# Kernel tuning notes

Measured on AMD Instinct MI355X. Metric: run time of the kernel, lower is better.

The kernel has to match this reference:

```python
import jax, jax.numpy as jnp
import numpy as np

B, S, D = 8, 2048, 512
KD = 64          # key_dim == value_dim
WIDTH = 128      # attention_width
NEG = 1.0e9


def setup_inputs() -> dict:
    key = jax.random.key(0)
    ks = jax.random.split(key, 16)
    glorot_dd = float(np.sqrt(6.0 / (D + KD)))
    glorot_sd = float(np.sqrt(6.0 / (S + KD)))
    u = lambda k, shape, lim: jax.random.uniform(k, shape, jnp.float32, -lim, lim)
    return {
        "x": jax.random.normal(ks[0], (B, S, D), jnp.float32),
        "Wqr": u(ks[1], (D, KD), glorot_dd), "bqr": jnp.zeros((KD,), jnp.float32),
        "Wqi": u(ks[2], (D, KD), glorot_dd), "bqi": jnp.zeros((KD,), jnp.float32),
        "Wkr": u(ks[3], (D, KD), glorot_dd), "bkr": jnp.zeros((KD,), jnp.float32),
        "Wki": u(ks[4], (D, KD), glorot_dd), "bki": jnp.zeros((KD,), jnp.float32),
        "Wv": u(ks[5], (D, KD), glorot_dd),  "bv": jnp.zeros((KD,), jnp.float32),
        "pos_qr": u(ks[6], (S, KD), glorot_sd), "pos_qi": u(ks[7], (S, KD), glorot_sd),
        "pos_kr": u(ks[8], (S, KD), glorot_sd), "pos_ki": u(ks[9], (S, KD), glorot_sd),
        "temperature": jnp.ones((1,), jnp.float32),
    }


def _masks():
    ind = jnp.arange(S)
    band = (jnp.abs(ind[:, None] - ind[None, :]) <= WIDTH).astype(jnp.float32)  # [S,S]
    causal = jnp.tril(jnp.ones((S, S), jnp.float32))                            # [S,S]
    return band, causal


def reference(x, Wqr, bqr, Wqi, bqi, Wkr, bkr, Wki, bki, Wv, bv,
              pos_qr, pos_qi, pos_kr, pos_ki, temperature):
    scale = 1.0 / jnp.sqrt(jnp.float32(KD))
    # complex Q/K via two real Dense layers; Q scaled BEFORE adding interference
    qr = (x @ Wqr + bqr) * scale + pos_qr[None]   # [B,S,KD]
    qi = (x @ Wqi + bqi) * scale + pos_qi[None]
    kr = (x @ Wkr + bkr) + pos_kr[None]
    ki = (x @ Wki + bki) + pos_ki[None]
    v = x @ Wv + bv                                # [B,S,KD]
    # real part of complex Q @ K^T (transpose, not conjugate-transpose)
    scores = (jnp.einsum('bsd,btd->bst', qr, kr)
              - jnp.einsum('bsd,btd->bst', qi, ki)) * scale  # [B,S,S]
    band, causal = _masks()
    scores = scores * band - NEG * (1.0 - band)
    scores = scores * causal - NEG * (1.0 - causal)
    probs = jax.nn.softmax(scores * temperature[0], axis=-1)
    return jnp.einsum('bst,btd->bsd', probs, v)
```

## Files before the change

kernel.cpp:

```cpp
#include <hip/hip_runtime.h>

#define NB 8
#define NS 2048
#define ND 512
#define NKD 64
#define NM (NB*NS)

typedef _Float16 f16x8 __attribute__((ext_vector_type(8)));
typedef float f32x4 __attribute__((ext_vector_type(4)));


__global__ __launch_bounds__(256) void wprep_kernel(
    const float* __restrict__ w0, const float* __restrict__ w1,
    const float* __restrict__ w2, const float* __restrict__ w3,
    const float* __restrict__ w4,
    f16x8* __restrict__ wfrag)
{
    const int t = blockIdx.x * 256 + threadIdx.x;
    const int p    = t >> 12;
    const int nf   = (t >> 10) & 3;
    const int kt   = (t >> 6) & 15;
    const int lane = t & 63;
    const float* __restrict__ W = (p==0)?w0:(p==1)?w1:(p==2)?w2:(p==3)?w3:w4;
    const int n  = nf*16 + (lane & 15);
    const int k0 = kt*32 + (lane >> 4)*8;
    f16x8 v;
    #pragma unroll
    for (int j = 0; j < 8; ++j)
        v[j] = (_Float16)W[(size_t)(k0 + j)*NKD + n];
    wfrag[t] = v;
}

__global__ __launch_bounds__(256) void proj_mfma(
    const float* __restrict__ x,
    const f16x8* __restrict__ wfrag,
    const float* __restrict__ b0, const float* __restrict__ b1,
    const float* __restrict__ b2, const float* __restrict__ b3,
    const float* __restrict__ b4,
    const float* __restrict__ p0, const float* __restrict__ p1,
    const float* __restrict__ p2, const float* __restrict__ p3,
    _Float16* __restrict__ qkri,
    _Float16* __restrict__ vT)
{
    const int g    = (blockIdx.x * 256 + threadIdx.x) >> 6;
    const int lane = threadIdx.x & 63;
    const int m0   = g * 16;

    const int row = m0 + (lane & 15);
    const int kb  = (lane >> 4) * 8;
    const float* __restrict__ xrow = x + (size_t)row * ND + kb;
    const f16x8* __restrict__ wf   = wfrag + lane;

    f32x4 acc[5][4];
    #pragma unroll
    for (int p = 0; p < 5; ++p)
        #pragma unroll
        for (int nf = 0; nf < 4; ++nf) acc[p][nf] = (f32x4){0.f,0.f,0.f,0.f};

    for (int kt = 0; kt < 16; ++kt) {
        float4 xa = *(const float4*)(xrow + kt*32);
        float4 xb = *(const float4*)(xrow + kt*32 + 4);
        f16x8 a;
        a[0]=(_Float16)xa.x; a[1]=(_Float16)xa.y;
        a[2]=(_Float16)xa.z; a[3]=(_Float16)xa.w;
        a[4]=(_Float16)xb.x; a[5]=(_Float16)xb.y;
        a[6]=(_Float16)xb.z; a[7]=(_Float16)xb.w;
        #pragma unroll
        for (int p = 0; p < 5; ++p)
            #pragma unroll
            for (int nf = 0; nf < 4; ++nf) {
                f16x8 b = wf[(p*4 + nf)*1024 + kt*64];
                acc[p][nf] = __builtin_amdgcn_mfma_f32_16x16x32_f16(a, b, acc[p][nf], 0, 0, 0);
            }
    }

    const float* biases[5] = {b0, b1, b2, b3, b4};
    const float* poss[4]   = {p0, p1, p2, p3};

    const int col   = lane & 15;
    const int rbase = (lane >> 4) << 2;
    const int bidx  = m0 >> 11;

    #pragma unroll
    for (int p = 0; p < 4; ++p) {
        _Float16* ob = qkri + ((size_t)p*NM + m0) * NKD;
        #pragma unroll
        for (int nf = 0; nf < 4; ++nf) {
            const int c = nf*16 + col;
            const float bb = biases[p][c];
            #pragma unroll
            for (int r = 0; r < 4; ++r) {
                const int mm = rbase + r;
                const int s  = (m0 + mm) & (NS - 1);
                float t = acc[p][nf][r] + bb;
                if (p < 2) t = t * 0.125f + poss[p][s*NKD + c];
                else       t = t + poss[p][s*NKD + c];
                ob[(size_t)mm*NKD + c] = (_Float16)t;
            }
        }
    }
    {
        _Float16* vb = vT + (size_t)bidx*NKD*NS;
        #pragma unroll
        for (int nf = 0; nf < 4; ++nf) {
            const int c = nf*16 + col;
            const float bb = b4[c];
            #pragma unroll
            for (int r = 0; r < 4; ++r) {
                const int s = (m0 + rbase + r) & (NS - 1);
                vb[(size_t)c*NS + s] = (_Float16)(acc[4][nf][r] + bb);
            }
        }
    }
}

#define SST 164
#define OST 68

__global__ __launch_bounds__(256) void attn_mfma(
    const _Float16* __restrict__ qkri,
    const _Float16* __restrict__ vT,
    const float* __restrict__ temp,
    float* __restrict__ out)
{
    __shared__ __align__(16) float scf[16*SST];
    __shared__ __align__(16) float olds[3][16*OST];

    const int tid  = threadIdx.x;
    const int w    = tid >> 6;
    const int lane = tid & 63;
    const int i0   = blockIdx.x * 16;
    const int b    = blockIdx.y;
    const int jb   = i0 - 128;

    const _Float16* __restrict__ qr_g = qkri + ((size_t)0*NM + (size_t)b*NS)*NKD;
    const _Float16* __restrict__ qi_g = qkri + ((size_t)1*NM + (size_t)b*NS)*NKD;
    const _Float16* __restrict__ kr_g = qkri + ((size_t)2*NM + (size_t)b*NS)*NKD;
    const _Float16* __restrict__ ki_g = qkri + ((size_t)3*NM + (size_t)b*NS)*NKD;
    const _Float16* __restrict__ vT_b = vT + (size_t)b*NKD*NS;

    const f16x8 zf = {};
    const int col  = lane & 15;
    const int seg  = lane >> 4;
    const int qg4  = seg * 4;

    const int qrow = i0 + col;
    const int d0   = seg * 8;
    f16x8 aqr[2], aqi[2];
    #pragma unroll
    for (int kt = 0; kt < 2; ++kt) {
        aqr[kt] = *(const f16x8*)&qr_g[(size_t)qrow*NKD + kt*32 + d0];
        f16x8 qi8 = *(const f16x8*)&qi_g[(size_t)qrow*NKD + kt*32 + d0];
        aqi[kt] = -qi8;
    }

    const float sT  = 0.125f * temp[0];
    const int jrmin = -jb;
    const int tA = (w == 0) ? 0 : (2*w + 1);
    const int tB = 2*w + 2;

    for (int t = tA; t <= tB; ++t) {
        const int row = jb + 16*t + col;
        const bool ok = (row >= 0);
        const _Float16* krp = kr_g + (size_t)row*NKD + d0;
        const _Float16* kip = ki_g + (size_t)row*NKD + d0;
        f16x8 bkr0 = ok ? *(const f16x8*)(krp)      : zf;
        f16x8 bkr1 = ok ? *(const f16x8*)(krp + 32) : zf;
        f16x8 bki0 = ok ? *(const f16x8*)(kip)      : zf;
        f16x8 bki1 = ok ? *(const f16x8*)(kip + 32) : zf;
        f32x4 acc = (f32x4){0.f,0.f,0.f,0.f};
        acc = __builtin_amdgcn_mfma_f32_16x16x32_f16(aqr[0], bkr0, acc, 0,0,0);
        acc = __builtin_amdgcn_mfma_f32_16x16x32_f16(aqr[1], bkr1, acc, 0,0,0);
        acc = __builtin_amdgcn_mfma_f32_16x16x32_f16(aqi[0], bki0, acc, 0,0,0);
        acc = __builtin_amdgcn_mfma_f32_16x16x32_f16(aqi[1], bki1, acc, 0,0,0);
        const int jr = 16*t + col;
        #pragma unroll
        for (int r = 0; r < 4; ++r) {
            const int row16 = qg4 + r;
            const bool okm = (jr >= row16) && (jr <= 128 + row16) && (jr >= jrmin);
            scf[(qg4 + r)*SST + jr] = okm ? acc[r]*sT : -1e30f;
        }
    }
    if (w == 0) {
        #pragma unroll
        for (int r = 0; r < 4; ++r)
            scf[(qg4 + r)*SST + 144 + col] = -1e30f;
    }
    __syncthreads();

    const float* srow = &scf[col*SST + seg*40];
    float4 vv[10];
    float m = -3e38f;
    #pragma unroll
    for (int c = 0; c < 10; ++c) {
        vv[c] = *(const float4*)(srow + 4*c);
        m = fmaxf(m, fmaxf(fmaxf(vv[c].x, vv[c].y), fmaxf(vv[c].z, vv[c].w)));
    }
    m = fmaxf(m, __shfl_xor(m, 16));
    m = fmaxf(m, __shfl_xor(m, 32));
    float l = 0.f;
    #pragma unroll
    for (int c = 0; c < 10; ++c) {
        l += __expf(vv[c].x - m) + __expf(vv[c].y - m)
           + __expf(vv[c].z - m) + __expf(vv[c].w - m);
    }
    l += __shfl_xor(l, 16);
    l += __shfl_xor(l, 32);
    const float inv = 1.0f / l;

    f32x4 oacc[4];
    #pragma unroll
    for (int nf = 0; nf < 4; ++nf) oacc[nf] = (f32x4){0.f,0.f,0.f,0.f};

    #pragma unroll
    for (int pass = 0; pass < 2; ++pass) {
        const int kt = (pass == 0) ? w : 4;
        if (pass == 1 && w != 0) break;
        const int sb = 32*kt + seg*8;
        float4 e0 = *(const float4*)&scf[col*SST + sb];
        float4 e1 = *(const float4*)&scf[col*SST + sb + 4];
        f16x8 a;
        a[0] = (_Float16)(__expf(e0.x - m) * inv);
        a[1] = (_Float16)(__expf(e0.y - m) * inv);
        a[2] = (_Float16)(__expf(e0.z - m) * inv);
        a[3] = (_Float16)(__expf(e0.w - m) * inv);
        a[4] = (_Float16)(__expf(e1.x - m) * inv);
        a[5] = (_Float16)(__expf(e1.y - m) * inv);
        a[6] = (_Float16)(__expf(e1.z - m) * inv);
        a[7] = (_Float16)(__expf(e1.w - m) * inv);
        const int k0 = jb + 32*kt + seg*8;
        const bool okv = (k0 >= 0) && (k0 <= NS - 8);
        #pragma unroll
        for (int nf = 0; nf < 4; ++nf) {
            const int d = nf*16 + col;
            f16x8 bv = okv ? *(const f16x8*)&vT_b[(size_t)d*NS + k0] : zf;
            oacc[nf] = __builtin_amdgcn_mfma_f32_16x16x32_f16(a, bv, oacc[nf], 0,0,0);
        }
    }

    if (w > 0) {
        #pragma unroll
        for (int nf = 0; nf < 4; ++nf)
            #pragma unroll
            for (int r = 0; r < 4; ++r)
                olds[w-1][(qg4 + r)*OST + nf*16 + col] = oacc[nf][r];
    }
    __syncthreads();
    if (w == 0) {
        float* ob = out + ((size_t)b*NS + i0)*NKD;
        #pragma unroll
        for (int nf = 0; nf < 4; ++nf)
            #pragma unroll
            for (int r = 0; r < 4; ++r) {
                const int idx = (qg4 + r)*OST + nf*16 + col;
                const float v = oacc[nf][r] + olds[0][idx] + olds[1][idx] + olds[2][idx];
                ob[(size_t)(qg4 + r)*NKD + nf*16 + col] = v;
            }
    }
}

extern "C" void kernel_launch(void* const* d_in, const int* in_sizes, int n_in,
                              void* d_out, int out_size, void* d_ws, size_t ws_size,
                              hipStream_t stream)
{
    const float* x    = (const float*)d_in[0];
    const float* w0   = (const float*)d_in[1];
    const float* b0   = (const float*)d_in[2];
    const float* w1   = (const float*)d_in[3];
    const float* b1   = (const float*)d_in[4];
    const float* w2   = (const float*)d_in[5];
    const float* b2   = (const float*)d_in[6];
    const float* w3   = (const float*)d_in[7];
    const float* b3   = (const float*)d_in[8];
    const float* w4   = (const float*)d_in[9];
    const float* b4   = (const float*)d_in[10];
    const float* p0   = (const float*)d_in[11];
    const float* p1   = (const float*)d_in[12];
    const float* p2   = (const float*)d_in[13];
    const float* p3   = (const float*)d_in[14];
    const float* temp = (const float*)d_in[15];

    char* ws = (char*)d_ws;
    f16x8*    wfrag = (f16x8*)ws;
    _Float16* qkri  = (_Float16*)(ws + 327680);
    _Float16* vT    = (_Float16*)(ws + 327680 + 8388608);

    wprep_kernel<<<80, 256, 0, stream>>>(w0, w1, w2, w3, w4, wfrag);

    proj_mfma<<<256, 256, 0, stream>>>(x, wfrag,
                                       b0, b1, b2, b3, b4,
                                       p0, p1, p2, p3, qkri, vT);

    dim3 gB(NS/16, NB);
    attn_mfma<<<gB, 256, 0, stream>>>(qkri, vT, temp, (float*)d_out);
}
```

Before: 43.77 us.

## Split projection outputs across wave pairs and stage V transpose through LDS

Each 16-row tile is now handled by two waves, each computing two of the four Q/K projections plus half of V. This halves per-wave accumulators and MFMA work and doubles the grid to 512 blocks for more parallelism. The V outputs are written to a shared-memory tile and then stored to vT as contiguous 16-byte vectors, replacing scattered 2-byte transposed stores. In exchange, x is loaded and converted twice per tile, and the block gains LDS use and a barrier.

```diff
diff --git a/kernel.cpp b/kernel.cpp
--- a/kernel.cpp
+++ b/kernel.cpp
@@ -42,20 +42,28 @@
     _Float16* __restrict__ qkri,
     _Float16* __restrict__ vT)
 {
-    const int g    = (blockIdx.x * 256 + threadIdx.x) >> 6;
+    __shared__ __align__(16) _Float16 vtile[64][40];
+
+    const int w    = threadIdx.x >> 6;
     const int lane = threadIdx.x & 63;
-    const int m0   = g * 16;
-
-    const int row = m0 + (lane & 15);
-    const int kb  = (lane >> 4) * 8;
-    const float* __restrict__ xrow = x + (size_t)row * ND + kb;
+    const int half = w & 1;
+    const int mt   = blockIdx.x*2 + (w >> 1);
+    const int m0   = mt * 16;
+
+    const int col   = lane & 15;
+    const int rbase = (lane >> 4) << 2;
+
+    const float* __restrict__ xrow = x + (size_t)(m0 + col) * ND + (lane >> 4)*8;
     const f16x8* __restrict__ wf   = wfrag + lane;
-
-    f32x4 acc[5][4];
-    #pragma unroll
-    for (int p = 0; p < 5; ++p)
-        #pragma unroll
-        for (int nf = 0; nf < 4; ++nf) acc[p][nf] = (f32x4){0.f,0.f,0.f,0.f};
+    const int pa = half * 2;
+
+    f32x4 acc[2][4], accv[2];
+    #pragma unroll
+    for (int pp = 0; pp < 2; ++pp)
+        #pragma unroll
+        for (int nf = 0; nf < 4; ++nf) acc[pp][nf] = (f32x4){0.f,0.f,0.f,0.f};
+    accv[0] = (f32x4){0.f,0.f,0.f,0.f};
+    accv[1] = (f32x4){0.f,0.f,0.f,0.f};
 
     for (int kt = 0; kt < 16; ++kt) {
         float4 xa = *(const float4*)(xrow + kt*32);
@@ -66,23 +74,26 @@
         a[4]=(_Float16)xb.x; a[5]=(_Float16)xb.y;
         a[6]=(_Float16)xb.z; a[7]=(_Float16)xb.w;
         #pragma unroll
-        for (int p = 0; p < 5; ++p)
+        for (int pp = 0; pp < 2; ++pp)
             #pragma unroll
             for (int nf = 0; nf < 4; ++nf) {
-                f16x8 b = wf[(p*4 + nf)*1024 + kt*64];
-                acc[p][nf] = __builtin_amdgcn_mfma_f32_16x16x32_f16(a, b, acc[p][nf], 0, 0, 0);
+                f16x8 b = wf[((pa + pp)*4 + nf)*1024 + kt*64];
+                acc[pp][nf] = __builtin_amdgcn_mfma_f32_16x16x32_f16(a, b, acc[pp][nf], 0, 0, 0);
             }
+        #pragma unroll
+        for (int j = 0; j < 2; ++j) {
+            const int nfv = half*2 + j;
+            f16x8 b = wf[(16 + nfv)*1024 + kt*64];
+            accv[j] = __builtin_amdgcn_mfma_f32_16x16x32_f16(a, b, accv[j], 0, 0, 0);
+        }
     }
 
     const float* biases[5] = {b0, b1, b2, b3, b4};
     const float* poss[4]   = {p0, p1, p2, p3};
 
-    const int col   = lane & 15;
-    const int rbase = (lane >> 4) << 2;
-    const int bidx  = m0 >> 11;
-
-    #pragma unroll
-    for (int p = 0; p < 4; ++p) {
+    #pragma unroll
+    for (int pp = 0; pp < 2; ++pp) {
+        const int p = pa + pp;
         _Float16* ob = qkri + ((size_t)p*NM + m0) * NKD;
         #pragma unroll
         for (int nf = 0; nf < 4; ++nf) {
@@ -92,25 +103,34 @@
             for (int r = 0; r < 4; ++r) {
                 const int mm = rbase + r;
                 const int s  = (m0 + mm) & (NS - 1);
-                float t = acc[p][nf][r] + bb;
+                float t = acc[pp][nf][r] + bb;
                 if (p < 2) t = t * 0.125f + poss[p][s*NKD + c];
                 else       t = t + poss[p][s*NKD + c];
                 ob[(size_t)mm*NKD + c] = (_Float16)t;
             }
         }
     }
+
+    #pragma unroll
+    for (int j = 0; j < 2; ++j) {
+        const int c = (half*2 + j)*16 + col;
+        const float bb = b4[c];
+        #pragma unroll
+        for (int r = 0; r < 4; ++r) {
+            const int sl = (w >> 1)*16 + rbase + r;
+            vtile[c][sl] = (_Float16)(accv[j][r] + bb);
+        }
+    }
+    __syncthreads();
     {
-        _Float16* vb = vT + (size_t)bidx*NKD*NS;
-        #pragma unroll
-        for (int nf = 0; nf < 4; ++nf) {
-            const int c = nf*16 + col;
-            const float bb = b4[c];
-            #pragma unroll
-            for (int r = 0; r < 4; ++r) {
-                const int s = (m0 + rbase + r) & (NS - 1);
-                vb[(size_t)c*NS + s] = (_Float16)(acc[4][nf][r] + bb);
-            }
-        }
+        const int t   = threadIdx.x;
+        const int d   = t >> 2;
+        const int sc  = (t & 3) * 8;
+        const int mblk = blockIdx.x * 32;
+        const int bidx = mblk >> 11;
+        const int sb   = mblk & (NS - 1);
+        f16x8 vv = *(const f16x8*)&vtile[d][sc];
+        *(f16x8*)&vT[((size_t)bidx*NKD + d)*NS + sb + sc] = vv;
     }
 }
 
@@ -287,7 +307,7 @@
 
     wprep_kernel<<<80, 256, 0, stream>>>(w0, w1, w2, w3, w4, wfrag);
 
-    proj_mfma<<<256, 256, 0, stream>>>(x, wfrag,
+    proj_mfma<<<512, 256, 0, stream>>>(x, wfrag,
                                        b0, b1, b2, b3, b4,
                                        p0, p1, p2, p3, qkri, vT);
 
```

Result: no change. 43.71 us (-0.1%).
